# Optimization experiments

Hardware: AMD Instinct MI355X
Metric: run time of the kernel (lower is better)

The kernel has to match this reference:

```python
import jax, jax.numpy as jnp
import numpy as np

# dims
B_, DM, DI, DS, DTR, DT_, G_, E_, K_, DC = 512, 1024, 2048, 64, 64, 64, 8, 4, 2, 4
# B_ batch, DM d_model, DI d_inner (expand*d_model), DS d_state, DTR dt_rank,
# DT_ D_time, G_ KAN grid size, E_ num_experts, K_ top_k, DC d_conv


def setup_inputs() -> dict:
    key = jax.random.key(0)
    ks = jax.random.split(key, 16)
    def n(i, shape, s=0.02):
        return jax.random.normal(ks[i], shape, dtype=jnp.float32) * s
    return {
        "uk_current_input": jax.random.normal(ks[0], (B_, DM), dtype=jnp.float32),
        "tk_current": jax.random.uniform(ks[1], (B_, 1), dtype=jnp.float32),
        "tk_previous": jax.random.uniform(ks[2], (B_, 1), dtype=jnp.float32),
        # input_proj
        "W_in": n(3, (DM, DM)), "b_in": jnp.zeros((DM,), jnp.float32),
        # K_MOTE router + sinusoidal time experts
        "router_W": n(4, (E_, 1), 1.0), "router_b": jnp.zeros((E_,), jnp.float32),
        "freq": jax.random.uniform(ks[5], (E_, DT_), minval=0.1, maxval=10.0),
        "phase": n(6, (E_, DT_), 1.0),
        "kan_W": n(7, (DT_, DT_, G_), 0.1),
        # Mamba SSM params
        "W_inproj": n(8, (2 * DI, DM)),
        "conv_w": n(9, (DI, DC), 0.1), "conv_b": jnp.zeros((DI,), jnp.float32),
        "W_x": n(10, (DTR + 2 * DS, DI)),
        "W_dt": n(11, (DI, DTR)), "dt_bias": jnp.full((DI,), -4.0, jnp.float32),
        "W_delta": n(12, (DI, DT_)),
        "A_log": jnp.log(jnp.tile(jnp.arange(1, DS + 1, dtype=jnp.float32), (DI, 1))),
        "D_skip": jnp.ones((DI,), jnp.float32),
        "W_out": n(13, (DM, DI)),
    }


def _k_mote(t, router_W, router_b, freq, phase):
    # t: (B,1) -> embedding (B, D_time), weights (B,E), mask (B,E)
    logits = t @ router_W.T + router_b                      # (B,E)
    w = jax.nn.softmax(logits, axis=-1)
    _, top_idx = jax.lax.top_k(w, K_)
    mask = jax.nn.one_hot(top_idx, E_, dtype=w.dtype).sum(axis=1)  # (B,E) binary
    w_sel = w * mask
    w_norm = w_sel / (w_sel.sum(axis=-1, keepdims=True) + 1e-8)
    # expert sinusoidal embeddings: (B,E,D_time)
    emb = jnp.sin(t[:, :, None] * freq[None] + phase[None])
    out = jnp.einsum('be,bed->bd', w_norm, emb)
    return out, w, mask


def _kan(x, kan_W):
    # rkhs_gaussian basis on fixed grid in [-1,1]
    grid = jnp.linspace(-1.0, 1.0, G_, dtype=x.dtype)
    h = 2.0 / (G_ - 1)
    phi = jnp.exp(-jnp.square((x[..., None] - grid) / h))   # (B, D_time, G)
    return jnp.einsum('big,oig->bo', phi, kan_W)


def _mamba_step(u, dt_emb, W_inproj, conv_w, conv_b, W_x, W_dt, dt_bias,
                W_delta, A_log, D_skip, W_out):
    # single-timestep selective scan (seq_len=1, zero initial state)
    xz = u @ W_inproj.T                                     # (B, 2*DI)
    x, z = jnp.split(xz, 2, axis=-1)
    # causal depthwise conv over a length-1 sequence with zero left-pad:
    # only the last kernel tap contributes
    x = x * conv_w[:, -1] + conv_b
    x = jax.nn.silu(x)
    x_dbl = x @ W_x.T                                       # (B, DTR+2*DS)
    dt_r = x_dbl[:, :DTR]
    Bmat = x_dbl[:, DTR:DTR + DS]                           # (B, DS)
    Cmat = x_dbl[:, DTR + DS:]                              # (B, DS)
    # dt modulated by the K-MOTE/KAN delta-time embedding
    dt = jax.nn.softplus(dt_r @ W_dt.T + dt_emb @ W_delta.T + dt_bias)  # (B, DI)
    # h_prev = 0 so exp(dt*A)*h_prev vanishes; h = (dt*B) * x
    h = (dt * x)[:, :, None] * Bmat[:, None, :]             # (B, DI, DS)
    y = jnp.einsum('bds,bs->bd', h, Cmat) + D_skip * x
    y = y * jax.nn.silu(z)
    return y @ W_out.T                                      # (B, DM)


def reference(uk_current_input, tk_current, tk_previous, W_in, b_in,
              router_W, router_b, freq, phase, kan_W, W_inproj, conv_w, conv_b,
              W_x, W_dt, dt_bias, W_delta, A_log, D_skip, W_out):
    processed_uk = uk_current_input @ W_in.T + b_in
    emb_tk, expert_weights, expert_mask = _k_mote(tk_current, router_W, router_b, freq, phase)
    emb_tk_prev, _, _ = _k_mote(tk_previous, router_W, router_b, freq, phase)
    delta_t_emb = _kan(emb_tk, kan_W) - _kan(emb_tk_prev, kan_W)
    hk = _mamba_step(processed_uk, delta_t_emb, W_inproj, conv_w, conv_b,
                     W_x, W_dt, dt_bias, W_delta, A_log, D_skip, W_out)
    return hk, expert_weights, expert_mask
```

## Files before the change

kernel.cpp:

```cpp
#include <hip/hip_runtime.h>
#include <hip/hip_bf16.h>
#include <math.h>

#define B_  512
#define DM  1024
#define DI  2048
#define DS  64
#define DTR 64
#define DT  64
#define G_  8
#define E_  4
#define DC  4

typedef __bf16 bf16x8 __attribute__((ext_vector_type(8)));
typedef float  f32x4  __attribute__((ext_vector_type(4)));
typedef unsigned short ushort_t;

__device__ __forceinline__ float bf2f(__hip_bfloat16 h) { return __bfloat162float(h); }
__device__ __forceinline__ __hip_bfloat16 f2bf(float f) { return __float2bfloat16(f); }
__device__ __forceinline__ float sigmoidf_(float x){ return 1.f/(1.f+expf(-x)); }
__device__ __forceinline__ float siluf_(float x){ return x*sigmoidf_(x); }
__device__ __forceinline__ float softplusf_(float x){ return (x>20.f)? x : log1pf(expf(x)); }

__device__ __forceinline__ unsigned int pack2(float a, float b) {
  unsigned short ua = __builtin_bit_cast(unsigned short, (__bf16)a);
  unsigned short ub = __builtin_bit_cast(unsigned short, (__bf16)b);
  return (unsigned int)ua | ((unsigned int)ub << 16);
}
__device__ __forceinline__ uint4 cvt8(float4 v0, float4 v1) {
  uint4 r;
  r.x = pack2(v0.x, v0.y); r.y = pack2(v0.z, v0.w);
  r.z = pack2(v1.x, v1.y); r.w = pack2(v1.z, v1.w);
  return r;
}

enum EpiKind { EPI_PART=0, EPI_G2=1, EPI_G4=2, EPI_BIAS=3 };

struct KParams {
  const float *uk, *tk_c, *tk_p, *W_in, *b_in, *rW, *rb, *freq, *phase, *kanW;
  const float *W_inproj, *conv_w, *conv_b, *W_x, *W_dt, *dt_bias, *W_delta, *D_skip, *W_out;
  __hip_bfloat16 *Pu, *Xs, *Sz, *Yb, *Acat;
  float *bc, *Part, *out_hk, *out_w, *out_mask;
};

template<int BM, int EK, bool CVTA, bool CVTB, bool B2>
__device__ __forceinline__ void gemm_tile(char* smemc, int bxi, int byi, int bzi,
    const void* __restrict__ Ap, const void* __restrict__ Bp, void* __restrict__ Coutp,
    int Ka, int Kb, int kLen, int N, const KParams& p)
{
  constexpr int BN = 64, BK = 64, SA = 72;
  constexpr int NA = (BM*BK)/(256*8);
  constexpr int NB = (BN*BK)/(256*8);
  constexpr int WMT = (BM/2)/16;
  constexpr int WNT = (BN/2)/16;
  ushort_t* sA = (ushort_t*)smemc;
  ushort_t* sB = (ushort_t*)(smemc + (size_t)2*BM*SA*sizeof(ushort_t));
  const int tid  = threadIdx.x;
  const int wave = tid >> 6, lane = tid & 63;
  const int wm = wave >> 1, wn = wave & 1;
  const int r = lane & 15, q = lane >> 4;
  const int bm = byi * BM, bn = bxi * BN;
  const int kBase = bzi * kLen;
  const int T = kLen / BK;

  float4 fa[NA][2]; uint4 ua[NA];
  float4 fb[NB][2]; uint4 ub[NB];

  auto loadTiles = [&](int k0) {
    #pragma unroll
    for (int c=0;c<NA;++c) {
      int idx = tid*8 + c*2048; int row = idx>>6, kk = idx&63;
      if constexpr (CVTA) {
        const float* s = (const float*)Ap + (size_t)(bm+row)*Ka + k0 + kk;
        fa[c][0] = *reinterpret_cast<const float4*>(s);
        fa[c][1] = *reinterpret_cast<const float4*>(s+4);
      } else {
        const __hip_bfloat16* s = (const __hip_bfloat16*)Ap + (size_t)(bm+row)*Ka + k0 + kk;
        ua[c] = *reinterpret_cast<const uint4*>(s);
      }
    }
    #pragma unroll
    for (int c=0;c<NB;++c) {
      int idx = tid*8 + c*2048; int row = idx>>6, kk = idx&63;
      if constexpr (B2) {
        const float* bb = (k0==0) ? (const float*)Bp : p.W_delta;
        const float* s = bb + (size_t)(bn+row)*Kb + kk;
        fb[c][0] = *reinterpret_cast<const float4*>(s);
        fb[c][1] = *reinterpret_cast<const float4*>(s+4);
      } else if constexpr (CVTB) {
        const float* s = (const float*)Bp + (size_t)(bn+row)*Kb + k0 + kk;
        fb[c][0] = *reinterpret_cast<const float4*>(s);
        fb[c][1] = *reinterpret_cast<const float4*>(s+4);
      } else {
        const __hip_bfloat16* s = (const __hip_bfloat16*)Bp + (size_t)(bn+row)*Kb + k0 + kk;
        ub[c] = *reinterpret_cast<const uint4*>(s);
      }
    }
  };
  auto writeTiles = [&](int buf) {
    #pragma unroll
    for (int c=0;c<NA;++c) {
      int idx = tid*8 + c*2048; int row = idx>>6, kk = idx&63;
      uint4 v; if constexpr (CVTA) v = cvt8(fa[c][0], fa[c][1]); else v = ua[c];
      *reinterpret_cast<uint4*>(&sA[buf*(BM*SA) + row*SA + kk]) = v;
    }
    #pragma unroll
    for (int c=0;c<NB;++c) {
      int idx = tid*8 + c*2048; int row = idx>>6, kk = idx&63;
      uint4 v; if constexpr (CVTB || B2) v = cvt8(fb[c][0], fb[c][1]); else v = ub[c];
      *reinterpret_cast<uint4*>(&sB[buf*(BN*SA) + row*SA + kk]) = v;
    }
  };

  f32x4 acc[WMT][WNT];
  #pragma unroll
  for (int i=0;i<WMT;++i)
    #pragma unroll
    for (int j=0;j<WNT;++j) acc[i][j] = (f32x4){0.f,0.f,0.f,0.f};

  loadTiles(kBase);
  writeTiles(0);
  for (int t=0; t<T; ++t) {
    __syncthreads();
    const int cur = t & 1;
    if (t+1 < T) loadTiles(kBase + (t+1)*BK);
    #pragma unroll
    for (int ks=0; ks<2; ++ks) {
      bf16x8 af[WMT], bfr[WNT];
      #pragma unroll
      for (int mt=0; mt<WMT; ++mt)
        af[mt] = *reinterpret_cast<const bf16x8*>(&sA[cur*(BM*SA) + (wm*(BM/2)+mt*16+r)*SA + ks*32 + q*8]);
      #pragma unroll
      for (int nt=0; nt<WNT; ++nt)
        bfr[nt] = *reinterpret_cast<const bf16x8*>(&sB[cur*(BN*SA) + (wn*(BN/2)+nt*16+r)*SA + ks*32 + q*8]);
      #pragma unroll
      for (int mt=0; mt<WMT; ++mt)
        #pragma unroll
        for (int nt=0; nt<WNT; ++nt)
          acc[mt][nt] = __builtin_amdgcn_mfma_f32_16x16x32_bf16(af[mt], bfr[nt], acc[mt][nt], 0,0,0);
    }
    if (t+1 < T) writeTiles(cur ^ 1);
  }

  #pragma unroll
  for (int mt=0; mt<WMT; ++mt) {
    #pragma unroll
    for (int nt=0; nt<WNT; ++nt) {
      #pragma unroll
      for (int i=0;i<4;++i) {
        int grow = bm + wm*(BM/2) + mt*16 + q*4 + i;
        int gcol = bn + wn*(BN/2) + nt*16 + r;
        float v = acc[mt][nt][i];
        if constexpr (EK == EPI_PART) {
          float* P = (float*)Coutp + (size_t)bzi * ((size_t)B_*N);
          P[(size_t)grow*N + gcol] = v;
        } else if constexpr (EK == EPI_BIAS) {
          p.Pu[(size_t)grow*N + gcol] = f2bf(v + p.b_in[gcol]);
        } else if constexpr (EK == EPI_G2) {
          if (gcol < DI) {
            float xc = v * p.conv_w[gcol*DC + (DC-1)] + p.conv_b[gcol];
            p.Xs[(size_t)grow*DI + gcol] = f2bf(siluf_(xc));
          } else {
            p.Sz[(size_t)grow*DI + (gcol - DI)] = f2bf(siluf_(v));
          }
        } else {
          float dt  = softplusf_(v + p.dt_bias[gcol]);
          float xsv = bf2f(p.Xs[(size_t)grow*DI + gcol]);
          float szv = bf2f(p.Sz[(size_t)grow*DI + gcol]);
          float y = (dt * xsv * p.bc[grow] + p.D_skip[gcol] * xsv) * szv;
          p.Yb[(size_t)grow*DI + gcol] = f2bf(y);
        }
      }
    }
  }
}


__device__ __forceinline__ void route(float t, const float* rW, const float* rb,
                                      float* w, float* mask, float* wn)
{
  float l[E_];
  float m = -1e30f;
  for (int e=0;e<E_;++e){ l[e] = t*rW[e] + rb[e]; m = fmaxf(m, l[e]); }
  float s = 0.f;
  for (int e=0;e<E_;++e){ w[e] = expf(l[e]-m); s += w[e]; }
  for (int e=0;e<E_;++e) w[e] /= s;
  int i1 = 0;
  for (int e=1;e<E_;++e) if (w[e] > w[i1]) i1 = e;
  int i2 = -1;
  for (int e=0;e<E_;++e) if (e != i1 && (i2 < 0 || w[e] > w[i2])) i2 = e;
  float ssel = w[i1] + w[i2] + 1e-8f;
  for (int e=0;e<E_;++e){
    float mk = (e==i1 || e==i2) ? 1.f : 0.f;
    mask[e] = mk;
    wn[e] = mk * w[e] / ssel;
  }
}

__device__ __forceinline__ void kan_job(char* smemc, int job, const KParams& p)
{
  float* dphi = (float*)smemc;
  const int wv = threadIdx.x >> 6, lane = threadIdx.x & 63;
  const int b = job*4 + wv;
  {
    float t  = p.tk_c[b];
    float tp = p.tk_p[b];
    float w_c[E_], mk_c[E_], wn_c[E_];
    float w_p[E_], mk_p[E_], wn_p[E_];
    route(t,  p.rW, p.rb, w_c, mk_c, wn_c);
    route(tp, p.rW, p.rb, w_p, mk_p, wn_p);
    if (lane < E_) {
      p.out_w[b*E_ + lane]    = w_c[lane];
      p.out_mask[b*E_ + lane] = mk_c[lane];
    }
    float ec = 0.f, epv = 0.f;
    #pragma unroll
    for (int e=0;e<E_;++e) {
      float f  = p.freq[e*DT + lane];
      float ph = p.phase[e*DT + lane];
      ec  += wn_c[e] * sinf(t*f + ph);
      epv += wn_p[e] * sinf(tp*f + ph);
    }
    const float h = 2.f/(G_-1);
    #pragma unroll
    for (int g=0; g<G_; ++g) {
      float gr = -1.f + g*h;
      float a  = (ec - gr)/h;
      float bb = (epv - gr)/h;
      dphi[wv*512 + lane*G_ + g] = expf(-a*a) - expf(-bb*bb);
    }
  }
  __syncthreads();
  {
    float accv = 0.f;
    const float* kw = p.kanW + (size_t)lane*(DT*G_);
    const float* dd = dphi + wv*512;
    #pragma unroll 4
    for (int j=0;j<DT*G_;j+=4) {
      float4 kv = *reinterpret_cast<const float4*>(kw + j);
      float4 dv = *reinterpret_cast<const float4*>(dd + j);
      accv += kv.x*dv.x + kv.y*dv.y + kv.z*dv.z + kv.w*dv.w;
    }
    p.Acat[b*128 + 64 + lane] = f2bf(accv);
  }
}


__global__ __launch_bounds__(256)
void g1kan_kernel(KParams p)
{
  __shared__ __align__(16) char smem[(2*32*72 + 2*64*72)*2];
  const int id = blockIdx.x;
  if (id < 256) {
    const int byi = id & 15, bxi = id >> 4;
    gemm_tile<32,EPI_BIAS,true,true,false>(smem, bxi, byi, 0,
        p.uk, p.W_in, nullptr, DM, DM, DM, DM, p);
  } else {
    kan_job(smem, id - 256, p);
  }
}

template<int BM, int MT, int NT, int EK, bool CVTA, bool CVTB, bool B2>
__global__ __launch_bounds__(256)
void gemm_mfirst(const void* __restrict__ Ap, const void* __restrict__ Bp,
                 void* __restrict__ Coutp, int Ka, int Kb, int kLen, int N, KParams p)
{
  __shared__ __align__(16) char smem[(2*BM*72 + 2*64*72)*2];
  const int id = blockIdx.x;
  const int byi = id % MT;
  const int rem = id / MT;
  const int bxi = rem % NT;
  const int bzi = rem / NT;
  gemm_tile<BM,EK,CVTA,CVTB,B2>(smem, bxi, byi, bzi, Ap, Bp, Coutp, Ka, Kb, kLen, N, p);
}

__global__ __launch_bounds__(256)
void r3_kernel(KParams p)
{
  __shared__ float sbc[128];
  const int row = blockIdx.x, col = threadIdx.x;
  float s = 0.f;
  if (col < 192) {
    #pragma unroll
    for (int k=0;k<8;++k) s += p.Part[(size_t)k*((size_t)B_*192) + row*192 + col];
    if (col < 64) p.Acat[row*128 + col] = f2bf(s);
    else          sbc[col-64] = s;
  }
  __syncthreads();
  if (col < 64) {
    float pval = sbc[col] * sbc[col+64];
    #pragma unroll
    for (int off=32; off; off>>=1) pval += __shfl_down(pval, off);
    if (col == 0) p.bc[row] = pval;
  }
}

__global__ __launch_bounds__(256)
void reduce_plain_kernel(KParams p)
{
  const int i = blockIdx.x*256 + threadIdx.x;
  const int total = B_*DM/4;
  const float4* pp = (const float4*)p.Part;
  float4 s = pp[i];
  #pragma unroll
  for (int k=1;k<4;++k){ float4 t = pp[i + k*total]; s.x+=t.x; s.y+=t.y; s.z+=t.z; s.w+=t.w; }
  ((float4*)p.out_hk)[i] = s;
}

extern "C" void kernel_launch(void* const* d_in, const int* in_sizes, int n_in,
                              void* d_out, int out_size, void* d_ws, size_t ws_size,
                              hipStream_t stream)
{
  KParams p;
  p.uk       = (const float*)d_in[0];
  p.tk_c     = (const float*)d_in[1];
  p.tk_p     = (const float*)d_in[2];
  p.W_in     = (const float*)d_in[3];
  p.b_in     = (const float*)d_in[4];
  p.rW       = (const float*)d_in[5];
  p.rb       = (const float*)d_in[6];
  p.freq     = (const float*)d_in[7];
  p.phase    = (const float*)d_in[8];
  p.kanW     = (const float*)d_in[9];
  p.W_inproj = (const float*)d_in[10];
  p.conv_w   = (const float*)d_in[11];
  p.conv_b   = (const float*)d_in[12];
  p.W_x      = (const float*)d_in[13];
  p.W_dt     = (const float*)d_in[14];
  p.dt_bias  = (const float*)d_in[15];
  p.W_delta  = (const float*)d_in[16];
  p.D_skip   = (const float*)d_in[18];
  p.W_out    = (const float*)d_in[19];

  char* ws = (char*)d_ws;
  p.Pu   = (__hip_bfloat16*)(ws);
  p.Xs   = (__hip_bfloat16*)(ws + (size_t)(1<<20));
  p.Sz   = (__hip_bfloat16*)(ws + (size_t)3*(1<<20));
  p.Yb   = (__hip_bfloat16*)(ws + (size_t)5*(1<<20));
  p.Acat = (__hip_bfloat16*)(ws + (size_t)7*(1<<20));
  p.bc   = (float*)         (ws + (size_t)7*(1<<20) + (128<<10));
  p.Part = (float*)         (ws + (size_t)8*(1<<20));

  p.out_hk   = (float*)d_out;
  p.out_w    = p.out_hk + (size_t)B_*DM;
  p.out_mask = p.out_w  + (size_t)B_*E_;

  g1kan_kernel<<<dim3(384), 256, 0, stream>>>(p);

  gemm_mfirst<64,8,64,EPI_G2,false,true,false><<<dim3(512), 256, 0, stream>>>(
      p.Pu, p.W_inproj, nullptr, DM, DM, DM, 2*DI, p);

  gemm_mfirst<32,16,3,EPI_PART,false,true,false><<<dim3(384), 256, 0, stream>>>(
      p.Xs, p.W_x, p.Part, DI, DI, 256, 192, p);

  r3_kernel<<<dim3(512), 256, 0, stream>>>(p);

  gemm_mfirst<32,16,32,EPI_G4,false,true,true><<<dim3(512), 256, 0, stream>>>(
      p.Acat, p.W_dt, nullptr, 128, 64, 128, DI, p);

  gemm_mfirst<32,16,16,EPI_PART,false,true,false><<<dim3(1024), 256, 0, stream>>>(
      p.Yb, p.W_out, p.Part, DI, DI, 512, DM, p);

  reduce_plain_kernel<<<dim3(512), 256, 0, stream>>>(p);
}
```

Measured before the change: 188.6 us.

## Fuse partial reductions into dt GEMM, widen tiles, drop split-K on out-proj

```diff
diff --git a/kernel.cpp b/kernel.cpp
--- a/kernel.cpp
+++ b/kernel.cpp
@@ -34,7 +34,7 @@
   return r;
 }
 
-enum EpiKind { EPI_PART=0, EPI_G2=1, EPI_G4=2, EPI_BIAS=3 };
+enum EpiKind { EPI_PART=0, EPI_G2=1, EPI_BIAS=3 };
 
 struct KParams {
   const float *uk, *tk_c, *tk_p, *W_in, *b_in, *rW, *rb, *freq, *phase, *kanW;
@@ -43,16 +43,15 @@
   float *bc, *Part, *out_hk, *out_w, *out_mask;
 };
 
-template<int BM, int EK, bool CVTA, bool CVTB, bool B2>
+template<int BM, int BN, int WMT, int WNT, int EK, bool CVTA, bool CVTB>
 __device__ __forceinline__ void gemm_tile(char* smemc, int bxi, int byi, int bzi,
     const void* __restrict__ Ap, const void* __restrict__ Bp, void* __restrict__ Coutp,
     int Ka, int Kb, int kLen, int N, const KParams& p)
 {
-  constexpr int BN = 64, BK = 64, SA = 72;
+  static_assert(BM == 32*WMT && BN == 32*WNT, "2x2 wave layout");
+  constexpr int BK = 64, SA = 72;
   constexpr int NA = (BM*BK)/(256*8);
   constexpr int NB = (BN*BK)/(256*8);
-  constexpr int WMT = (BM/2)/16;
-  constexpr int WNT = (BN/2)/16;
   ushort_t* sA = (ushort_t*)smemc;
   ushort_t* sB = (ushort_t*)(smemc + (size_t)2*BM*SA*sizeof(ushort_t));
   const int tid  = threadIdx.x;
@@ -82,12 +81,7 @@
     #pragma unroll
     for (int c=0;c<NB;++c) {
       int idx = tid*8 + c*2048; int row = idx>>6, kk = idx&63;
-      if constexpr (B2) {
-        const float* bb = (k0==0) ? (const float*)Bp : p.W_delta;
-        const float* s = bb + (size_t)(bn+row)*Kb + kk;
-        fb[c][0] = *reinterpret_cast<const float4*>(s);
-        fb[c][1] = *reinterpret_cast<const float4*>(s+4);
-      } else if constexpr (CVTB) {
+      if constexpr (CVTB) {
         const float* s = (const float*)Bp + (size_t)(bn+row)*Kb + k0 + kk;
         fb[c][0] = *reinterpret_cast<const float4*>(s);
         fb[c][1] = *reinterpret_cast<const float4*>(s+4);
@@ -107,7 +101,7 @@
     #pragma unroll
     for (int c=0;c<NB;++c) {
       int idx = tid*8 + c*2048; int row = idx>>6, kk = idx&63;
-      uint4 v; if constexpr (CVTB || B2) v = cvt8(fb[c][0], fb[c][1]); else v = ub[c];
+      uint4 v; if constexpr (CVTB) v = cvt8(fb[c][0], fb[c][1]); else v = ub[c];
       *reinterpret_cast<uint4*>(&sB[buf*(BN*SA) + row*SA + kk]) = v;
     }
   };
@@ -129,10 +123,10 @@
       bf16x8 af[WMT], bfr[WNT];
       #pragma unroll
       for (int mt=0; mt<WMT; ++mt)
-        af[mt] = *reinterpret_cast<const bf16x8*>(&sA[cur*(BM*SA) + (wm*(BM/2)+mt*16+r)*SA + ks*32 + q*8]);
+        af[mt] = *reinterpret_cast<const bf16x8*>(&sA[cur*(BM*SA) + (wm*(WMT*16)+mt*16+r)*SA + ks*32 + q*8]);
       #pragma unroll
       for (int nt=0; nt<WNT; ++nt)
-        bfr[nt] = *reinterpret_cast<const bf16x8*>(&sB[cur*(BN*SA) + (wn*(BN/2)+nt*16+r)*SA + ks*32 + q*8]);
+        bfr[nt] = *reinterpret_cast<const bf16x8*>(&sB[cur*(BN*SA) + (wn*(WNT*16)+nt*16+r)*SA + ks*32 + q*8]);
       #pragma unroll
       for (int mt=0; mt<WMT; ++mt)
         #pragma unroll
@@ -148,8 +142,8 @@
     for (int nt=0; nt<WNT; ++nt) {
       #pragma unroll
       for (int i=0;i<4;++i) {
-        int grow = bm + wm*(BM/2) + mt*16 + q*4 + i;
-        int gcol = bn + wn*(BN/2) + nt*16 + r;
+        int grow = bm + wm*(WMT*16) + mt*16 + q*4 + i;
+        int gcol = bn + wn*(WNT*16) + nt*16 + r;
         float v = acc[mt][nt][i];
         if constexpr (EK == EPI_PART) {
           float* P = (float*)Coutp + (size_t)bzi * ((size_t)B_*N);
@@ -163,12 +157,6 @@
           } else {
             p.Sz[(size_t)grow*DI + (gcol - DI)] = f2bf(siluf_(v));
           }
-        } else {
-          float dt  = softplusf_(v + p.dt_bias[gcol]);
-          float xsv = bf2f(p.Xs[(size_t)grow*DI + gcol]);
-          float szv = bf2f(p.Sz[(size_t)grow*DI + gcol]);
-          float y = (dt * xsv * p.bc[grow] + p.D_skip[gcol] * xsv) * szv;
-          p.Yb[(size_t)grow*DI + gcol] = f2bf(y);
         }
       }
     }
@@ -249,62 +237,126 @@
 __global__ __launch_bounds__(256)
 void g1kan_kernel(KParams p)
 {
-  __shared__ __align__(16) char smem[(2*32*72 + 2*64*72)*2];
+  __shared__ __align__(16) char smem[(2*32*72 + 2*128*72)*2];
   const int id = blockIdx.x;
-  if (id < 256) {
-    const int byi = id & 15, bxi = id >> 4;
-    gemm_tile<32,EPI_BIAS,true,true,false>(smem, bxi, byi, 0,
+  if (id < 128) {
+    const int byi = id % 16, bxi = id / 16;
+    gemm_tile<32,128,1,4,EPI_BIAS,true,true>(smem, bxi, byi, 0,
         p.uk, p.W_in, nullptr, DM, DM, DM, DM, p);
   } else {
-    kan_job(smem, id - 256, p);
-  }
-}
-
-template<int BM, int MT, int NT, int EK, bool CVTA, bool CVTB, bool B2>
+    kan_job(smem, id - 128, p);
+  }
+}
+
+template<int BM, int BN, int WMT, int WNT, int MT, int NT, int EK, bool CVTA, bool CVTB>
 __global__ __launch_bounds__(256)
 void gemm_mfirst(const void* __restrict__ Ap, const void* __restrict__ Bp,
                  void* __restrict__ Coutp, int Ka, int Kb, int kLen, int N, KParams p)
 {
-  __shared__ __align__(16) char smem[(2*BM*72 + 2*64*72)*2];
+  __shared__ __align__(16) char smem[(2*BM*72 + 2*BN*72)*2];
   const int id = blockIdx.x;
   const int byi = id % MT;
   const int rem = id / MT;
   const int bxi = rem % NT;
   const int bzi = rem / NT;
-  gemm_tile<BM,EK,CVTA,CVTB,B2>(smem, bxi, byi, bzi, Ap, Bp, Coutp, Ka, Kb, kLen, N, p);
+  gemm_tile<BM,BN,WMT,WNT,EK,CVTA,CVTB>(smem, bxi, byi, bzi, Ap, Bp, Coutp, Ka, Kb, kLen, N, p);
 }
 
 __global__ __launch_bounds__(256)
-void r3_kernel(KParams p)
-{
-  __shared__ float sbc[128];
-  const int row = blockIdx.x, col = threadIdx.x;
-  float s = 0.f;
-  if (col < 192) {
-    #pragma unroll
-    for (int k=0;k<8;++k) s += p.Part[(size_t)k*((size_t)B_*192) + row*192 + col];
-    if (col < 64) p.Acat[row*128 + col] = f2bf(s);
-    else          sbc[col-64] = s;
+void g4_kernel(KParams p)
+{
+  __shared__ __align__(16) ushort_t sA4[32*136];
+  __shared__ __align__(16) ushort_t sB4[128*136];
+  __shared__ float sBcOut[32];
+  float* sBC = (float*)sB4;
+
+  const int tid = threadIdx.x;
+  const int byi = blockIdx.x % 16, bxi = blockIdx.x / 16;
+  const int bm = byi*32, bn = bxi*128;
+
+  #pragma unroll
+  for (int c=0;c<6;++c) {
+    int f4id = tid + c*256;
+    int row = f4id / 48, cq = f4id % 48;
+    int col0 = cq*4;
+    const float* src = p.Part + (size_t)(bm+row)*192 + col0;
+    float4 s = {0.f,0.f,0.f,0.f};
+    #pragma unroll
+    for (int k=0;k<8;++k) {
+      float4 t = *reinterpret_cast<const float4*>(src + (size_t)k*((size_t)B_*192));
+      s.x+=t.x; s.y+=t.y; s.z+=t.z; s.w+=t.w;
+    }
+    if (col0 < 64) {
+      uint2 o; o.x = pack2(s.x, s.y); o.y = pack2(s.z, s.w);
+      *reinterpret_cast<uint2*>(&sA4[row*136 + col0]) = o;
+    } else {
+      *reinterpret_cast<float4*>(&sBC[row*128 + (col0-64)]) = s;
+    }
+  }
+  {
+    int row = tid >> 3, c0 = (tid & 7)*8;
+    uint4 kv = *reinterpret_cast<const uint4*>(p.Acat + (size_t)(bm+row)*128 + 64 + c0);
+    *reinterpret_cast<uint4*>(&sA4[row*136 + 64 + c0]) = kv;
   }
   __syncthreads();
-  if (col < 64) {
-    float pval = sbc[col] * sbc[col+64];
-    #pragma unroll
-    for (int off=32; off; off>>=1) pval += __shfl_down(pval, off);
-    if (col == 0) p.bc[row] = pval;
-  }
-}
-
-__global__ __launch_bounds__(256)
-void reduce_plain_kernel(KParams p)
-{
-  const int i = blockIdx.x*256 + threadIdx.x;
-  const int total = B_*DM/4;
-  const float4* pp = (const float4*)p.Part;
-  float4 s = pp[i];
-  #pragma unroll
-  for (int k=1;k<4;++k){ float4 t = pp[i + k*total]; s.x+=t.x; s.y+=t.y; s.z+=t.z; s.w+=t.w; }
-  ((float4*)p.out_hk)[i] = s;
+
+  if (tid < 64) {
+    int row = tid >> 1, half = tid & 1;
+    const float* base = &sBC[row*128 + half*32];
+    float a = 0.f;
+    #pragma unroll
+    for (int j=0;j<8;++j) {
+      float4 bv = *reinterpret_cast<const float4*>(base + 4*j);
+      float4 cv = *reinterpret_cast<const float4*>(base + 64 + 4*j);
+      a += bv.x*cv.x + bv.y*cv.y + bv.z*cv.z + bv.w*cv.w;
+    }
+    a += __shfl_xor(a, 1);
+    if (half == 0) sBcOut[row] = a;
+  }
+  __syncthreads();
+
+  #pragma unroll
+  for (int c=0;c<8;++c) {
+    int e = tid + c*256;
+    int row = e >> 4, col0 = (e & 15)*8;
+    const float* src = (col0 < 64) ? (p.W_dt   + (size_t)(bn+row)*64 + col0)
+                                   : (p.W_delta+ (size_t)(bn+row)*64 + (col0-64));
+    float4 v0 = *reinterpret_cast<const float4*>(src);
+    float4 v1 = *reinterpret_cast<const float4*>(src+4);
+    *reinterpret_cast<uint4*>(&sB4[row*136 + col0]) = cvt8(v0, v1);
+  }
+  __syncthreads();
+
+  const int wave = tid >> 6, lane = tid & 63;
+  const int wm = wave >> 1, wn = wave & 1;
+  const int r = lane & 15, q = lane >> 4;
+  f32x4 acc[4];
+  #pragma unroll
+  for (int nt=0;nt<4;++nt) acc[nt] = (f32x4){0.f,0.f,0.f,0.f};
+  #pragma unroll
+  for (int ks=0;ks<4;++ks) {
+    bf16x8 af = *reinterpret_cast<const bf16x8*>(&sA4[(wm*16+r)*136 + ks*32 + q*8]);
+    #pragma unroll
+    for (int nt=0;nt<4;++nt) {
+      bf16x8 bf = *reinterpret_cast<const bf16x8*>(&sB4[(wn*64+nt*16+r)*136 + ks*32 + q*8]);
+      acc[nt] = __builtin_amdgcn_mfma_f32_16x16x32_bf16(af, bf, acc[nt], 0,0,0);
+    }
+  }
+
+  #pragma unroll
+  for (int nt=0;nt<4;++nt) {
+    #pragma unroll
+    for (int i=0;i<4;++i) {
+      int lrow = wm*16 + q*4 + i;
+      int grow = bm + lrow;
+      int gcol = bn + wn*64 + nt*16 + r;
+      float dt  = softplusf_(acc[nt][i] + p.dt_bias[gcol]);
+      float xsv = bf2f(p.Xs[(size_t)grow*DI + gcol]);
+      float szv = bf2f(p.Sz[(size_t)grow*DI + gcol]);
+      float y = (dt * xsv * sBcOut[lrow] + p.D_skip[gcol] * xsv) * szv;
+      p.Yb[(size_t)grow*DI + gcol] = f2bf(y);
+    }
+  }
 }
 
 extern "C" void kernel_launch(void* const* d_in, const int* in_sizes, int n_in,
@@ -345,21 +397,16 @@
   p.out_w    = p.out_hk + (size_t)B_*DM;
   p.out_mask = p.out_w  + (size_t)B_*E_;
 
-  g1kan_kernel<<<dim3(384), 256, 0, stream>>>(p);
-
-  gemm_mfirst<64,8,64,EPI_G2,false,true,false><<<dim3(512), 256, 0, stream>>>(
+  g1kan_kernel<<<dim3(256), 256, 0, stream>>>(p);
+
+  gemm_mfirst<64,128,2,4,8,32,EPI_G2,false,true><<<dim3(256), 256, 0, stream>>>(
       p.Pu, p.W_inproj, nullptr, DM, DM, DM, 2*DI, p);
 
-  gemm_mfirst<32,16,3,EPI_PART,false,true,false><<<dim3(384), 256, 0, stream>>>(
+  gemm_mfirst<32,64,1,2,16,3,EPI_PART,false,true><<<dim3(384), 256, 0, stream>>>(
       p.Xs, p.W_x, p.Part, DI, DI, 256, 192, p);
 
-  r3_kernel<<<dim3(512), 256, 0, stream>>>(p);
-
-  gemm_mfirst<32,16,32,EPI_G4,false,true,true><<<dim3(512), 256, 0, stream>>>(
-      p.Acat, p.W_dt, nullptr, 128, 64, 128, DI, p);
-
-  gemm_mfirst<32,16,16,EPI_PART,false,true,false><<<dim3(1024), 256, 0, stream>>>(
-      p.Yb, p.W_out, p.Part, DI, DI, 512, DM, p);
-
-  reduce_plain_kernel<<<dim3(512), 256, 0, stream>>>(p);
-}
+  g4_kernel<<<dim3(256), 256, 0, stream>>>(p);
+
+  gemm_mfirst<32,64,1,2,16,16,EPI_PART,false,true><<<dim3(256), 256, 0, stream>>>(
+      p.Yb, p.W_out, p.out_hk, DI, DI, DI, DM, p);
+}
```

Result: slower. 201.5 us (+6.8%).

## Pre-convert fp32 inputs and weights to bf16 in a separate pass before GEMMs

Applied to the files above, without the earlier changes.

```diff
diff --git a/kernel.cpp b/kernel.cpp
--- a/kernel.cpp
+++ b/kernel.cpp
@@ -34,25 +34,50 @@
   return r;
 }
 
-enum EpiKind { EPI_PART=0, EPI_G2=1, EPI_G4=2, EPI_BIAS=3 };
+enum EpiKind { EPI_PART=0, EPI_G2=1, EPI_G4=2 };
 
 struct KParams {
   const float *uk, *tk_c, *tk_p, *W_in, *b_in, *rW, *rb, *freq, *phase, *kanW;
   const float *W_inproj, *conv_w, *conv_b, *W_x, *W_dt, *dt_bias, *W_delta, *D_skip, *W_out;
   __hip_bfloat16 *Pu, *Xs, *Sz, *Yb, *Acat;
+  __hip_bfloat16 *uk_bf, *Win_bf, *Wip_bf, *Wx_bf, *Wdt128, *Wout_bf;
   float *bc, *Part, *out_hk, *out_w, *out_mask;
 };
 
-template<int BM, int EK, bool CVTA, bool CVTB, bool B2>
+__device__ __forceinline__ void cvt_chunk(const float* __restrict__ s,
+                                          __hip_bfloat16* __restrict__ d)
+{
+  float4 v0 = *reinterpret_cast<const float4*>(s);
+  float4 v1 = *reinterpret_cast<const float4*>(s + 4);
+  *reinterpret_cast<uint4*>(d) = cvt8(v0, v1);
+}
+
+__global__ __launch_bounds__(256)
+void convert_kernel(KParams p)
+{
+  const int id = blockIdx.x, t = threadIdx.x;
+  if (id < 256)       { size_t c = (size_t)id*256 + t;        cvt_chunk(p.uk      + c*8, p.uk_bf  + c*8); }
+  else if (id < 768)  { size_t c = (size_t)(id-256)*256 + t;  cvt_chunk(p.W_in    + c*8, p.Win_bf + c*8); }
+  else if (id < 2816) { size_t c = (size_t)(id-768)*256 + t;  cvt_chunk(p.W_inproj+ c*8, p.Wip_bf + c*8); }
+  else if (id < 3008) { size_t c = (size_t)(id-2816)*256 + t; cvt_chunk(p.W_x     + c*8, p.Wx_bf  + c*8); }
+  else if (id < 4032) { size_t c = (size_t)(id-3008)*256 + t; cvt_chunk(p.W_out   + c*8, p.Wout_bf+ c*8); }
+  else {               size_t c = (size_t)(id-4032)*256 + t;
+    int row = (int)(c >> 4), col0 = ((int)c & 15)*8;
+    const float* s = (col0 < 64) ? (p.W_dt    + (size_t)row*64 + col0)
+                                 : (p.W_delta + (size_t)row*64 + (col0-64));
+    cvt_chunk(s, p.Wdt128 + (size_t)row*128 + col0);
+  }
+}
+
+template<int BM, int BN, int WMT, int WNT, int EK>
 __device__ __forceinline__ void gemm_tile(char* smemc, int bxi, int byi, int bzi,
-    const void* __restrict__ Ap, const void* __restrict__ Bp, void* __restrict__ Coutp,
-    int Ka, int Kb, int kLen, int N, const KParams& p)
-{
-  constexpr int BN = 64, BK = 64, SA = 72;
+    const __hip_bfloat16* __restrict__ Ap, const __hip_bfloat16* __restrict__ Bp,
+    float* __restrict__ Coutp, int Ka, int Kb, int kLen, int N, const KParams& p)
+{
+  static_assert(BM == 32*WMT && BN == 32*WNT, "2x2 wave layout");
+  constexpr int BK = 64, SA = 72;
   constexpr int NA = (BM*BK)/(256*8);
   constexpr int NB = (BN*BK)/(256*8);
-  constexpr int WMT = (BM/2)/16;
-  constexpr int WNT = (BN/2)/16;
   ushort_t* sA = (ushort_t*)smemc;
   ushort_t* sB = (ushort_t*)(smemc + (size_t)2*BM*SA*sizeof(ushort_t));
   const int tid  = threadIdx.x;
@@ -63,52 +88,30 @@
   const int kBase = bzi * kLen;
   const int T = kLen / BK;
 
-  float4 fa[NA][2]; uint4 ua[NA];
-  float4 fb[NB][2]; uint4 ub[NB];
+  uint4 ua[NA], ub[NB];
 
   auto loadTiles = [&](int k0) {
     #pragma unroll
     for (int c=0;c<NA;++c) {
       int idx = tid*8 + c*2048; int row = idx>>6, kk = idx&63;
-      if constexpr (CVTA) {
-        const float* s = (const float*)Ap + (size_t)(bm+row)*Ka + k0 + kk;
-        fa[c][0] = *reinterpret_cast<const float4*>(s);
-        fa[c][1] = *reinterpret_cast<const float4*>(s+4);
-      } else {
-        const __hip_bfloat16* s = (const __hip_bfloat16*)Ap + (size_t)(bm+row)*Ka + k0 + kk;
-        ua[c] = *reinterpret_cast<const uint4*>(s);
-      }
+      ua[c] = *reinterpret_cast<const uint4*>(Ap + (size_t)(bm+row)*Ka + k0 + kk);
     }
     #pragma unroll
     for (int c=0;c<NB;++c) {
       int idx = tid*8 + c*2048; int row = idx>>6, kk = idx&63;
-      if constexpr (B2) {
-        const float* bb = (k0==0) ? (const float*)Bp : p.W_delta;
-        const float* s = bb + (size_t)(bn+row)*Kb + kk;
-        fb[c][0] = *reinterpret_cast<const float4*>(s);
-        fb[c][1] = *reinterpret_cast<const float4*>(s+4);
-      } else if constexpr (CVTB) {
-        const float* s = (const float*)Bp + (size_t)(bn+row)*Kb + k0 + kk;
-        fb[c][0] = *reinterpret_cast<const float4*>(s);
-        fb[c][1] = *reinterpret_cast<const float4*>(s+4);
-      } else {
-        const __hip_bfloat16* s = (const __hip_bfloat16*)Bp + (size_t)(bn+row)*Kb + k0 + kk;
-        ub[c] = *reinterpret_cast<const uint4*>(s);
-      }
+      ub[c] = *reinterpret_cast<const uint4*>(Bp + (size_t)(bn+row)*Kb + k0 + kk);
     }
   };
   auto writeTiles = [&](int buf) {
     #pragma unroll
     for (int c=0;c<NA;++c) {
       int idx = tid*8 + c*2048; int row = idx>>6, kk = idx&63;
-      uint4 v; if constexpr (CVTA) v = cvt8(fa[c][0], fa[c][1]); else v = ua[c];
-      *reinterpret_cast<uint4*>(&sA[buf*(BM*SA) + row*SA + kk]) = v;
+      *reinterpret_cast<uint4*>(&sA[buf*(BM*SA) + row*SA + kk]) = ua[c];
     }
     #pragma unroll
     for (int c=0;c<NB;++c) {
       int idx = tid*8 + c*2048; int row = idx>>6, kk = idx&63;
-      uint4 v; if constexpr (CVTB || B2) v = cvt8(fb[c][0], fb[c][1]); else v = ub[c];
-      *reinterpret_cast<uint4*>(&sB[buf*(BN*SA) + row*SA + kk]) = v;
+      *reinterpret_cast<uint4*>(&sB[buf*(BN*SA) + row*SA + kk]) = ub[c];
     }
   };
 
@@ -129,10 +132,10 @@
       bf16x8 af[WMT], bfr[WNT];
       #pragma unroll
       for (int mt=0; mt<WMT; ++mt)
-        af[mt] = *reinterpret_cast<const bf16x8*>(&sA[cur*(BM*SA) + (wm*(BM/2)+mt*16+r)*SA + ks*32 + q*8]);
+        af[mt] = *reinterpret_cast<const bf16x8*>(&sA[cur*(BM*SA) + (wm*(WMT*16)+mt*16+r)*SA + ks*32 + q*8]);
       #pragma unroll
       for (int nt=0; nt<WNT; ++nt)
-        bfr[nt] = *reinterpret_cast<const bf16x8*>(&sB[cur*(BN*SA) + (wn*(BN/2)+nt*16+r)*SA + ks*32 + q*8]);
+        bfr[nt] = *reinterpret_cast<const bf16x8*>(&sB[cur*(BN*SA) + (wn*(WNT*16)+nt*16+r)*SA + ks*32 + q*8]);
       #pragma unroll
       for (int mt=0; mt<WMT; ++mt)
         #pragma unroll
@@ -148,14 +151,12 @@
     for (int nt=0; nt<WNT; ++nt) {
       #pragma unroll
       for (int i=0;i<4;++i) {
-        int grow = bm + wm*(BM/2) + mt*16 + q*4 + i;
-        int gcol = bn + wn*(BN/2) + nt*16 + r;
+        int grow = bm + wm*(WMT*16) + mt*16 + q*4 + i;
+        int gcol = bn + wn*(WNT*16) + nt*16 + r;
         float v = acc[mt][nt][i];
         if constexpr (EK == EPI_PART) {
-          float* P = (float*)Coutp + (size_t)bzi * ((size_t)B_*N);
+          float* P = Coutp + (size_t)bzi * ((size_t)B_*N);
           P[(size_t)grow*N + gcol] = v;
-        } else if constexpr (EK == EPI_BIAS) {
-          p.Pu[(size_t)grow*N + gcol] = f2bf(v + p.b_in[gcol]);
         } else if constexpr (EK == EPI_G2) {
           if (gcol < DI) {
             float xc = v * p.conv_w[gcol*DC + (DC-1)] + p.conv_b[gcol];
@@ -251,44 +252,57 @@
 {
   __shared__ __align__(16) char smem[(2*32*72 + 2*64*72)*2];
   const int id = blockIdx.x;
-  if (id < 256) {
-    const int byi = id & 15, bxi = id >> 4;
-    gemm_tile<32,EPI_BIAS,true,true,false>(smem, bxi, byi, 0,
-        p.uk, p.W_in, nullptr, DM, DM, DM, DM, p);
+  if (id < 1024) {
+    const int bxi = id & 15, byi = (id >> 4) & 15, bzi = id >> 8;
+    gemm_tile<32,64,1,2,EPI_PART>(smem, bxi, byi, bzi,
+        p.uk_bf, p.Win_bf, p.Part, DM, DM, 256, DM, p);
   } else {
-    kan_job(smem, id - 256, p);
-  }
-}
-
-template<int BM, int MT, int NT, int EK, bool CVTA, bool CVTB, bool B2>
-__global__ __launch_bounds__(256)
-void gemm_mfirst(const void* __restrict__ Ap, const void* __restrict__ Bp,
-                 void* __restrict__ Coutp, int Ka, int Kb, int kLen, int N, KParams p)
-{
-  __shared__ __align__(16) char smem[(2*BM*72 + 2*64*72)*2];
+    kan_job(smem, id - 1024, p);
+  }
+}
+
+template<int BM, int BN, int WMT, int WNT, int NT, int MT, int EK>
+__global__ __launch_bounds__(256)
+void gemm_xfirst(const __hip_bfloat16* __restrict__ Ap, const __hip_bfloat16* __restrict__ Bp,
+                 float* __restrict__ Coutp, int Ka, int Kb, int kLen, int N, KParams p)
+{
+  __shared__ __align__(16) char smem[(2*BM*72 + 2*BN*72)*2];
   const int id = blockIdx.x;
-  const int byi = id % MT;
-  const int rem = id / MT;
-  const int bxi = rem % NT;
-  const int bzi = rem / NT;
-  gemm_tile<BM,EK,CVTA,CVTB,B2>(smem, bxi, byi, bzi, Ap, Bp, Coutp, Ka, Kb, kLen, N, p);
-}
-
-__global__ __launch_bounds__(256)
-void r3_kernel(KParams p)
-{
-  __shared__ float sbc[128];
+  const int bxi = id % NT;
+  const int rem = id / NT;
+  const int byi = rem % MT;
+  const int bzi = rem / MT;
+  gemm_tile<BM,BN,WMT,WNT,EK>(smem, bxi, byi, bzi, Ap, Bp, Coutp, Ka, Kb, kLen, N, p);
+}
+
+__global__ __launch_bounds__(256)
+void reduce_bias_kernel(KParams p)
+{
+  const int i = blockIdx.x*256 + threadIdx.x;
+  const int total = B_*DM/4;
+  const float4* pp = (const float4*)p.Part;
+  float4 s = pp[i];
+  #pragma unroll
+  for (int k=1;k<4;++k){ float4 t = pp[i + k*total]; s.x+=t.x; s.y+=t.y; s.z+=t.z; s.w+=t.w; }
+  float4 bv = ((const float4*)p.b_in)[i & (DM/4 - 1)];
+  uint2 o; o.x = pack2(s.x+bv.x, s.y+bv.y); o.y = pack2(s.z+bv.z, s.w+bv.w);
+  ((uint2*)p.Pu)[i] = o;
+}
+
+__global__ __launch_bounds__(192)
+void reduce_g3_kernel(KParams p)
+{
   const int row = blockIdx.x, col = threadIdx.x;
+  const int stride = B_*192;
   float s = 0.f;
-  if (col < 192) {
-    #pragma unroll
-    for (int k=0;k<8;++k) s += p.Part[(size_t)k*((size_t)B_*192) + row*192 + col];
-    if (col < 64) p.Acat[row*128 + col] = f2bf(s);
-    else          sbc[col-64] = s;
-  }
+  #pragma unroll
+  for (int k=0;k<8;++k) s += p.Part[(size_t)k*stride + row*192 + col];
+  __shared__ float sBC[128];
+  if (col < 64) p.Acat[row*128 + col] = f2bf(s);
+  else          sBC[col-64] = s;
   __syncthreads();
   if (col < 64) {
-    float pval = sbc[col] * sbc[col+64];
+    float pval = sBC[col] * sBC[col+64];
     #pragma unroll
     for (int off=32; off; off>>=1) pval += __shfl_down(pval, off);
     if (col == 0) p.bc[row] = pval;
@@ -333,33 +347,40 @@
   p.W_out    = (const float*)d_in[19];
 
   char* ws = (char*)d_ws;
-  p.Pu   = (__hip_bfloat16*)(ws);
-  p.Xs   = (__hip_bfloat16*)(ws + (size_t)(1<<20));
-  p.Sz   = (__hip_bfloat16*)(ws + (size_t)3*(1<<20));
-  p.Yb   = (__hip_bfloat16*)(ws + (size_t)5*(1<<20));
-  p.Acat = (__hip_bfloat16*)(ws + (size_t)7*(1<<20));
-  p.bc   = (float*)         (ws + (size_t)7*(1<<20) + (128<<10));
-  p.Part = (float*)         (ws + (size_t)8*(1<<20));
+  p.Pu     = (__hip_bfloat16*)(ws);
+  p.Xs     = (__hip_bfloat16*)(ws + (size_t)(1<<20));
+  p.Sz     = (__hip_bfloat16*)(ws + (size_t)3*(1<<20));
+  p.Yb     = (__hip_bfloat16*)(ws + (size_t)5*(1<<20));
+  p.Acat   = (__hip_bfloat16*)(ws + (size_t)7*(1<<20));
+  p.bc     = (float*)         (ws + (size_t)7*(1<<20) + (128<<10));
+  p.Part   = (float*)         (ws + (size_t)8*(1<<20));
+  p.uk_bf  = (__hip_bfloat16*)(ws + (size_t)16*(1<<20));
+  p.Win_bf = (__hip_bfloat16*)(ws + (size_t)17*(1<<20));
+  p.Wip_bf = (__hip_bfloat16*)(ws + (size_t)19*(1<<20));
+  p.Wx_bf  = (__hip_bfloat16*)(ws + (size_t)27*(1<<20));
+  p.Wdt128 = (__hip_bfloat16*)(ws + (size_t)28*(1<<20));
+  p.Wout_bf= (__hip_bfloat16*)(ws + (size_t)29*(1<<20));
 
   p.out_hk   = (float*)d_out;
   p.out_w    = p.out_hk + (size_t)B_*DM;
   p.out_mask = p.out_w  + (size_t)B_*E_;
 
-  g1kan_kernel<<<dim3(384), 256, 0, stream>>>(p);
-
-  gemm_mfirst<64,8,64,EPI_G2,false,true,false><<<dim3(512), 256, 0, stream>>>(
-      p.Pu, p.W_inproj, nullptr, DM, DM, DM, 2*DI, p);
-
-  gemm_mfirst<32,16,3,EPI_PART,false,true,false><<<dim3(384), 256, 0, stream>>>(
-      p.Xs, p.W_x, p.Part, DI, DI, 256, 192, p);
-
-  r3_kernel<<<dim3(512), 256, 0, stream>>>(p);
-
-  gemm_mfirst<32,16,32,EPI_G4,false,true,true><<<dim3(512), 256, 0, stream>>>(
-      p.Acat, p.W_dt, nullptr, 128, 64, 128, DI, p);
-
-  gemm_mfirst<32,16,16,EPI_PART,false,true,false><<<dim3(1024), 256, 0, stream>>>(
-      p.Yb, p.W_out, p.Part, DI, DI, 512, DM, p);
-
+  convert_kernel<<<dim3(4160), 256, 0, stream>>>(p);
+
+  g1kan_kernel<<<dim3(1152), 256, 0, stream>>>(p);
+  reduce_bias_kernel<<<dim3(512), 256, 0, stream>>>(p);
+
+  gemm_xfirst<32,64,1,2,64,16,EPI_G2><<<dim3(1024), 256, 0, stream>>>(
+      p.Pu, p.Wip_bf, nullptr, DM, DM, DM, 2*DI, p);
+
+  gemm_xfirst<32,64,1,2,3,16,EPI_PART><<<dim3(384), 256, 0, stream>>>(
+      p.Xs, p.Wx_bf, p.Part, DI, DI, 256, 192, p);
+  reduce_g3_kernel<<<dim3(512), 192, 0, stream>>>(p);
+
+  gemm_xfirst<32,64,1,2,32,16,EPI_G4><<<dim3(512), 256, 0, stream>>>(
+      p.Acat, p.Wdt128, nullptr, 128, 128, 128, DI, p);
+
+  gemm_xfirst<32,64,1,2,16,16,EPI_PART><<<dim3(1024), 256, 0, stream>>>(
+      p.Yb, p.Wout_bf, p.Part, DI, DI, 512, DM, p);
   reduce_plain_kernel<<<dim3(512), 256, 0, stream>>>(p);
 }
```

Result: slower. 225.1 us (+19.3%).
